# Optimization experiments

Measured on AMD Instinct MI355X. Metric: run time of the kernel, lower is better.

The kernel has to match this reference:

```python
import jax, jax.numpy as jnp
import numpy as np
import math

GROUPS = 32
HEADS = 8
EPS_GN = 1e-5


def group_norm(x, w, b):
    # x: [B, C, H, W]; GroupNorm32 computes in float32
    B, C, H, W = x.shape
    xg = x.astype(jnp.float32).reshape(B, GROUPS, C // GROUPS, H, W)
    mu = xg.mean(axis=(2, 3, 4), keepdims=True)
    var = xg.var(axis=(2, 3, 4), keepdims=True)
    xn = (xg - mu) * jax.lax.rsqrt(var + EPS_GN)
    xn = xn.reshape(B, C, H, W)
    return (xn * w[None, :, None, None] + b[None, :, None, None]).astype(x.dtype)


def fresnel_interference(H, W, wavelength):
    ys, xs = jnp.meshgrid(jnp.arange(H, dtype=jnp.float32),
                          jnp.arange(W, dtype=jnp.float32), indexing='ij')
    pos = jnp.stack([ys, xs], axis=-1).reshape(-1, 2)  # [N, 2]
    diff = pos[None, :, :] - pos[:, None, :]           # [N, N, 2]
    dist = jnp.sqrt((diff ** 2).sum(-1) + 1e-8)        # [N, N]
    phase = 2.0 * math.pi * dist / (jnp.abs(wavelength) * H + 1e-6)
    return jnp.cos(phase)


def fresnel_attn(h, qkv_w, out_w, out_b, wavelength):
    B, C, H, W = h.shape
    N = H * W
    dh = C // HEADS
    scale = dh ** -0.5
    xf = h.reshape(B, C, N).transpose(0, 2, 1)                 # [B, N, C]
    qkv = xf @ qkv_w                                            # [B, N, 3C]
    q, k, v = jnp.split(qkv, 3, axis=-1)
    def heads(t):
        return t.reshape(B, N, HEADS, dh).transpose(0, 2, 1, 3)  # [B, Hh, N, dh]
    q, k, v = heads(q), heads(k), heads(v)
    dots = jnp.einsum('bhnd,bhmd->bhnm', q, k) * scale
    interference = fresnel_interference(H, W, wavelength)       # [N, N]
    dots = dots + interference[None, None] * 0.1
    attn = jax.nn.softmax(dots, axis=-1)
    out = jnp.einsum('bhnm,bhmd->bhnd', attn, v)
    out = out.transpose(0, 2, 1, 3).reshape(B, N, C)
    out = out @ out_w + out_b
    return out.transpose(0, 2, 1).reshape(B, C, H, W)


def cross_attn(h, context, q_w, k_w, v_w, out_w, out_b):
    B, C, H, W = h.shape
    N = H * W
    inner = q_w.shape[1]
    dh = inner // HEADS
    scale = dh ** -0.5
    xf = h.reshape(B, C, N).transpose(0, 2, 1)                 # [B, N, C]
    q = xf @ q_w                                                # [B, N, inner]
    k = context @ k_w                                           # [B, L, inner]
    v = context @ v_w
    L = context.shape[1]
    q = q.reshape(B, N, HEADS, dh).transpose(0, 2, 1, 3)
    k = k.reshape(B, L, HEADS, dh).transpose(0, 2, 1, 3)
    v = v.reshape(B, L, HEADS, dh).transpose(0, 2, 1, 3)
    attn = jax.nn.softmax(jnp.einsum('bhnd,bhld->bhnl', q, k) * scale, axis=-1)
    out = jnp.einsum('bhnl,bhld->bhnd', attn, v)
    out = out.transpose(0, 2, 1, 3).reshape(B, N, inner)
    out = out @ out_w + out_b
    return out.transpose(0, 2, 1).reshape(B, C, H, W)


def setup_inputs() -> dict:
    key = jax.random.key(0)
    ks = jax.random.split(key, 10)
    B, C, H, W = 4, 512, 32, 32
    ctx_len, ctx_dim = 77, 768
    s = lambda d: 1.0 / math.sqrt(d)
    return {
        'x': jax.random.normal(ks[0], (B, C, H, W), jnp.float32),
        'context': jax.random.normal(ks[1], (B, ctx_len, ctx_dim), jnp.float32),
        'gn1_w': jnp.ones((C,), jnp.float32),
        'gn1_b': jnp.zeros((C,), jnp.float32),
        'gn2_w': jnp.ones((C,), jnp.float32),
        'gn2_b': jnp.zeros((C,), jnp.float32),
        'fa_qkv_w': jax.random.normal(ks[2], (C, 3 * C), jnp.float32) * s(C),
        'fa_out_w': jax.random.normal(ks[3], (C, C), jnp.float32) * s(C),
        'fa_out_b': jnp.zeros((C,), jnp.float32),
        'wavelength': jnp.asarray(0.1, jnp.float32),
        'ca_q_w': jax.random.normal(ks[4], (C, 512), jnp.float32) * s(C),
        'ca_k_w': jax.random.normal(ks[5], (ctx_dim, 512), jnp.float32) * s(ctx_dim),
        'ca_v_w': jax.random.normal(ks[6], (ctx_dim, 512), jnp.float32) * s(ctx_dim),
        'ca_out_w': jax.random.normal(ks[7], (512, C), jnp.float32) * s(512),
        'ca_out_b': jnp.zeros((C,), jnp.float32),
    }


def reference(x, context, gn1_w, gn1_b, gn2_w, gn2_b,
              fa_qkv_w, fa_out_w, fa_out_b, wavelength,
              ca_q_w, ca_k_w, ca_v_w, ca_out_w, ca_out_b):
    h = group_norm(x, gn1_w, gn1_b)
    h = fresnel_attn(h, fa_qkv_w, fa_out_w, fa_out_b, wavelength)
    x = x + h
    h = group_norm(x, gn2_w, gn2_b)
    h = cross_attn(h, context, ca_q_w, ca_k_w, ca_v_w, ca_out_w, ca_out_b)
    return x + h
```

## Files before the change

kernel.cpp:

```cpp
#include <hip/hip_runtime.h>
#include <hip/hip_bf16.h>
#include <math.h>

#define B_    4
#define N_    1024
#define L_    77

typedef float f4 __attribute__((ext_vector_type(4)));
typedef short bf8 __attribute__((ext_vector_type(8)));
typedef short s4v __attribute__((ext_vector_type(4)));

#if __has_builtin(__builtin_amdgcn_exp2f)
#define EXP2(x) __builtin_amdgcn_exp2f(x)
#else
#define EXP2(x) exp2f(x)
#endif

__device__ __forceinline__ float fs(short s) {
    unsigned u = ((unsigned)(unsigned short)s) << 16;
    return __builtin_bit_cast(float, u);
}
__device__ __forceinline__ short sf(float f) {
    unsigned u = __builtin_bit_cast(unsigned, f);
    unsigned r = (u + 0x7FFF + ((u >> 16) & 1)) >> 16;
    return (short)r;
}
__device__ __forceinline__ bf8 zero8() { bf8 v; for (int i = 0; i < 8; ++i) v[i] = 0; return v; }
__device__ __forceinline__ f4 zerof4() { f4 v; for (int i = 0; i < 4; ++i) v[i] = 0.f; return v; }

#define MFMA(a, b, c) __builtin_amdgcn_mfma_f32_16x16x32_bf16((a), (b), (c), 0, 0, 0)

__device__ __forceinline__ void gn_body(const float* __restrict__ src,
                                        const float* __restrict__ w,
                                        const float* __restrict__ bs,
                                        short* __restrict__ dst, int g, int b)
{
    const float* xb = src + ((size_t)b * 512 + g * 16) * 1024;
    float s = 0.f, ss = 0.f;
    for (int l = threadIdx.x; l < 4096; l += 256) {
        float4 v = *(const float4*)(xb + l * 4);
        s += v.x + v.y + v.z + v.w;
        ss += v.x * v.x + v.y * v.y + v.z * v.z + v.w * v.w;
    }
    for (int off = 32; off; off >>= 1) {
        s  += __shfl_down(s,  off);
        ss += __shfl_down(ss, off);
    }
    __shared__ float sred[8], ssred[8];
    int wid = threadIdx.x >> 6;
    if ((threadIdx.x & 63) == 0) { sred[wid] = s; ssred[wid] = ss; }
    __syncthreads();
    if (threadIdx.x == 0) {
        float S = 0.f, SS = 0.f;
        for (int i = 0; i < 4; ++i) { S += sred[i]; SS += ssred[i]; }
        float mu = S * (1.f / 16384.f);
        float var = SS * (1.f / 16384.f) - mu * mu;
        sred[4] = mu; ssred[4] = rsqrtf(var + 1e-5f);
    }
    __syncthreads();
    float mu = sred[4], rs = ssred[4];

    int c4 = threadIdx.x & 3, nb = threadIdx.x >> 2;
    int c = g * 16 + c4 * 4;
    float4 wv = *(const float4*)(w + c);
    float4 bv = *(const float4*)(bs + c);
    for (int rep = 0; rep < 16; ++rep) {
        int n = rep * 64 + nb;
        float v0 = xb[(size_t)(c4 * 4 + 0) * 1024 + n];
        float v1 = xb[(size_t)(c4 * 4 + 1) * 1024 + n];
        float v2 = xb[(size_t)(c4 * 4 + 2) * 1024 + n];
        float v3 = xb[(size_t)(c4 * 4 + 3) * 1024 + n];
        s4v hb;
        hb[0] = sf((v0 - mu) * rs * wv.x + bv.x);
        hb[1] = sf((v1 - mu) * rs * wv.y + bv.y);
        hb[2] = sf((v2 - mu) * rs * wv.z + bv.z);
        hb[3] = sf((v3 - mu) * rs * wv.w + bv.w);
        *(s4v*)(dst + ((size_t)b * 1024 + n) * 512 + c) = hb;
    }
}

__device__ __forceinline__ void wtile(const float* __restrict__ in, short* __restrict__ out,
                                      int K, int J, int tile, int tid, float (*t)[33])
{
    int jt = J >> 5;
    int j0 = (tile % jt) * 32, k0 = (tile / jt) * 32;
    int tx = tid & 31, ty = tid >> 5;
#pragma unroll
    for (int i = 0; i < 4; ++i)
        t[ty + i * 8][tx] = in[(size_t)(k0 + ty + i * 8) * J + j0 + tx];
    __syncthreads();
#pragma unroll
    for (int i = 0; i < 4; ++i)
        out[(size_t)(j0 + ty + i * 8) * K + k0 + tx] = sf(t[tx][ty + i * 8]);
}

__global__ __launch_bounds__(256)
void prep_mega(const float* __restrict__ x, const float* __restrict__ gn1w,
               const float* __restrict__ gn1b, short* __restrict__ h1b,
               const float* __restrict__ wl, short* __restrict__ tab,
               float* __restrict__ gstat,
               const float* __restrict__ qkvw, short* __restrict__ qkvwT,
               const float* __restrict__ faow, short* __restrict__ faowT,
               const float* __restrict__ caqw, short* __restrict__ caqwT,
               const float* __restrict__ cakw, short* __restrict__ cakwT,
               const float* __restrict__ cavw, short* __restrict__ cavwT,
               const float* __restrict__ caow, short* __restrict__ caowT,
               const float* __restrict__ ctx, short* __restrict__ ctxb)
{
    __shared__ float tls[32][33];
    int bid = blockIdx.x, tid = threadIdx.x;
    if (bid < 128) { gn_body(x, gn1w, gn1b, h1b, bid & 31, bid >> 5); return; }
    bid -= 128;
    if (bid < 16) {
        if (bid == 0) gstat[tid] = 0.f;
        int idx = bid * 256 + tid;
        if (idx < 3969) {
            int i = idx / 63, j = idx - i * 63;
            float dy = (float)(i - 31), dx = (float)(j - 31);
            float dist = sqrtf(dy * dy + dx * dx + 1e-8f);
            float den = fabsf(wl[0]) * 32.0f + 1e-6f;
            tab[idx] = sf(0.1f * cosf(6.283185307179586f * dist / den) * 1.4426950408889634f);
        }
        return;
    }
    bid -= 16;
    if (bid < 768) { wtile(qkvw, qkvwT, 512, 1536, bid, tid, tls); return; }
    bid -= 768;
    if (bid < 256) { wtile(faow, faowT, 512, 512, bid, tid, tls); return; }
    bid -= 256;
    if (bid < 256) { wtile(caqw, caqwT, 512, 512, bid, tid, tls); return; }
    bid -= 256;
    if (bid < 384) { wtile(cakw, cakwT, 768, 512, bid, tid, tls); return; }
    bid -= 384;
    if (bid < 384) { wtile(cavw, cavwT, 768, 512, bid, tid, tls); return; }
    bid -= 384;
    if (bid < 256) { wtile(caow, caowT, 512, 512, bid, tid, tls); return; }
    bid -= 256;
    int base = bid * 1024 + tid * 4;
    float4 v = *(const float4*)(ctx + base);
    s4v o; o[0] = sf(v.x); o[1] = sf(v.y); o[2] = sf(v.z); o[3] = sf(v.w);
    *(s4v*)(ctxb + base) = o;
}

__global__ __launch_bounds__(256)
void gn2_norm(const float* __restrict__ x1, const float* __restrict__ gstat,
              const float* __restrict__ w, const float* __restrict__ bs,
              short* __restrict__ dst)
{
    int g = blockIdx.x, b = blockIdx.y;
    float S  = gstat[b * 64 + g * 2];
    float SS = gstat[b * 64 + g * 2 + 1];
    float mu = S * (1.f / 16384.f);
    float var = SS * (1.f / 16384.f) - mu * mu;
    float rs = rsqrtf(var + 1e-5f);
    const float* xb = x1 + ((size_t)b * 512 + g * 16) * 1024;

    int c4 = threadIdx.x & 3, nb = threadIdx.x >> 2;
    int c = g * 16 + c4 * 4;
    float4 wv = *(const float4*)(w + c);
    float4 bv = *(const float4*)(bs + c);
    for (int rep = 0; rep < 16; ++rep) {
        int n = rep * 64 + nb;
        float v0 = xb[(size_t)(c4 * 4 + 0) * 1024 + n];
        float v1 = xb[(size_t)(c4 * 4 + 1) * 1024 + n];
        float v2 = xb[(size_t)(c4 * 4 + 2) * 1024 + n];
        float v3 = xb[(size_t)(c4 * 4 + 3) * 1024 + n];
        s4v hb;
        hb[0] = sf((v0 - mu) * rs * wv.x + bv.x);
        hb[1] = sf((v1 - mu) * rs * wv.y + bv.y);
        hb[2] = sf((v2 - mu) * rs * wv.z + bv.z);
        hb[3] = sf((v3 - mu) * rs * wv.w + bv.w);
        *(s4v*)(dst + ((size_t)b * 1024 + n) * 512 + c) = hb;
    }
}

template<int EPI>
__device__ __forceinline__ void gemm_body(
    short* As, short* Ws, int j0, int m0, int b,
    const short* __restrict__ A, const short* __restrict__ Wt,
    const float* __restrict__ bias, const float* __restrict__ res,
    void* __restrict__ outv, void* __restrict__ out2v, float* __restrict__ gstat,
    int M, int K, int J, long aStride, long wStride, long oStride, long o2Stride)
{
    int tid = threadIdx.x, w = tid >> 6, lane = tid & 63;
    int lr = lane & 15, lg = lane >> 4;
    int wr = w >> 1, wc = w & 1;
    const short* Ab  = A  + (size_t)b * aStride;
    const short* Wtb = Wt + (size_t)b * wStride;
    int r0 = tid >> 2, c0 = (tid & 3) * 8;
    bool gA0 = (m0 + r0) < M;
    const short* ap0 = Ab + (size_t)(m0 + r0) * K + c0;
    const short* wp0 = Wtb + (size_t)(j0 + r0) * K + c0;
    const short* wp1 = Wtb + (size_t)(j0 + 64 + r0) * K + c0;

    f4 acc[2][4];
#pragma unroll
    for (int i = 0; i < 2; ++i)
#pragma unroll
        for (int j = 0; j < 4; ++j) acc[i][j] = zerof4();

    *(bf8*)(As + r0 * 40 + c0) = gA0 ? *(const bf8*)ap0 : zero8();
    *(bf8*)(Ws + r0 * 40 + c0) = *(const bf8*)wp0;
    *(bf8*)(Ws + (64 + r0) * 40 + c0) = *(const bf8*)wp1;
    __syncthreads();

    int nk = K >> 5;
    for (int t = 0; t < nk; ++t) {
        int curA = (t & 1) * 2560, curW = (t & 1) * 5120;
        bool more = (t + 1) < nk;
        bf8 na0, nw0, nw1;
        if (more) {
            int ko = (t + 1) << 5;
            na0 = gA0 ? *(const bf8*)(ap0 + ko) : zero8();
            nw0 = *(const bf8*)(wp0 + ko);
            nw1 = *(const bf8*)(wp1 + ko);
        }
        bf8 af[2], bfr[4];
#pragma unroll
        for (int fi = 0; fi < 2; ++fi)
            af[fi] = *(const bf8*)(As + curA + (wr * 32 + fi * 16 + lr) * 40 + lg * 8);
#pragma unroll
        for (int fj = 0; fj < 4; ++fj)
            bfr[fj] = *(const bf8*)(Ws + curW + (wc * 64 + fj * 16 + lr) * 40 + lg * 8);
#pragma unroll
        for (int fi = 0; fi < 2; ++fi)
#pragma unroll
            for (int fj = 0; fj < 4; ++fj)
                acc[fi][fj] = MFMA(af[fi], bfr[fj], acc[fi][fj]);
        if (more) {
            int nbA = 2560 - curA, nbW = 5120 - curW;
            *(bf8*)(As + nbA + r0 * 40 + c0) = na0;
            *(bf8*)(Ws + nbW + r0 * 40 + c0) = nw0;
            *(bf8*)(Ws + nbW + (64 + r0) * 40 + c0) = nw1;
        }
        __syncthreads();
    }

    if (EPI == 1 || EPI == 2) {
        float* out = (float*)outv + (size_t)b * oStride;
        const float* rp = res + (size_t)b * oStride;
#pragma unroll
        for (int fi = 0; fi < 2; ++fi) {
            int mbase = m0 + wr * 32 + fi * 16 + lg * 4;
            float4 bq = *(const float4*)(bias + mbase);
            float bvr[4] = {bq.x, bq.y, bq.z, bq.w};
            float sg = 0.f, ssg = 0.f;
#pragma unroll
            for (int reg = 0; reg < 4; ++reg) {
                size_t ro = (size_t)(mbase + reg) * J + j0 + wc * 64;
#pragma unroll
                for (int fj = 0; fj < 4; ++fj) {
                    size_t idx = ro + fj * 16 + lr;
                    float v = acc[fi][fj][reg] + bvr[reg] + rp[idx];
                    out[idx] = v;
                    if (EPI == 2) { sg += v; ssg += v * v; }
                }
            }
            if (EPI == 2) {
#pragma unroll
                for (int off = 32; off; off >>= 1) {
                    sg  += __shfl_down(sg,  off);
                    ssg += __shfl_down(ssg, off);
                }
                if (lane == 0) {
                    int g = mbase >> 4;
                    atomicAdd(&gstat[b * 64 + g * 2], sg);
                    atomicAdd(&gstat[b * 64 + g * 2 + 1], ssg);
                }
            }
        }
    } else if (EPI == 3) {
        if (j0 < 1024) {
            short* out = (short*)outv + (size_t)b * oStride;
#pragma unroll
            for (int fi = 0; fi < 2; ++fi)
#pragma unroll
                for (int reg = 0; reg < 4; ++reg) {
                    int m = m0 + wr * 32 + fi * 16 + lg * 4 + reg;
#pragma unroll
                    for (int fj = 0; fj < 4; ++fj)
                        out[(size_t)m * 1024 + j0 + wc * 64 + fj * 16 + lr] = sf(acc[fi][fj][reg]);
                }
        } else {
            short* Vgp = (short*)out2v + (size_t)b * o2Stride;
#pragma unroll
            for (int fi = 0; fi < 2; ++fi) {
                int n = m0 + wr * 32 + fi * 16 + lg * 4;
#pragma unroll
                for (int fj = 0; fj < 4; ++fj) {
                    int dg = j0 - 1024 + wc * 64 + fj * 16 + lr;
                    s4v v;
#pragma unroll
                    for (int reg = 0; reg < 4; ++reg) v[reg] = sf(acc[fi][fj][reg]);
                    *(s4v*)(Vgp + (size_t)dg * 1024 + n) = v;
                }
            }
        }
    } else {
        if (j0 < 512) {
            short* out = (short*)outv + (size_t)b * oStride;
#pragma unroll
            for (int fi = 0; fi < 2; ++fi)
#pragma unroll
                for (int reg = 0; reg < 4; ++reg) {
                    int m = m0 + wr * 32 + fi * 16 + lg * 4 + reg;
                    if (m < M) {
#pragma unroll
                        for (int fj = 0; fj < 4; ++fj)
                            out[(size_t)m * 512 + j0 + wc * 64 + fj * 16 + lr] = sf(acc[fi][fj][reg]);
                    }
                }
        } else {
            short* vt = (short*)out2v + (size_t)b * o2Stride;
#pragma unroll
            for (int fi = 0; fi < 2; ++fi) {
                int l0 = m0 + wr * 32 + fi * 16 + lg * 4;
                if (l0 < 80) {
#pragma unroll
                    for (int fj = 0; fj < 4; ++fj) {
                        int dg = j0 - 512 + wc * 64 + fj * 16 + lr;
                        s4v v;
#pragma unroll
                        for (int reg = 0; reg < 4; ++reg) v[reg] = sf(acc[fi][fj][reg]);
                        *(s4v*)(vt + (size_t)dg * 80 + l0) = v;
                    }
                }
            }
        }
    }
}

template<int EPI>
__global__ __launch_bounds__(256)
void gemm_std(const short* __restrict__ A, const short* __restrict__ Wt,
              const float* __restrict__ bias, const float* __restrict__ res,
              void* __restrict__ outv, void* __restrict__ out2v, float* __restrict__ gstat,
              int M, int K, int J, long aStride, long wStride, long oStride, long o2Stride)
{
    __shared__ short As[2 * 64 * 40];
    __shared__ short Ws[2 * 128 * 40];
    gemm_body<EPI>(As, Ws, blockIdx.x * 128, blockIdx.y * 64, blockIdx.z,
                   A, Wt, bias, res, outv, out2v, gstat, M, K, J,
                   aStride, wStride, oStride, o2Stride);
}

__global__ __launch_bounds__(256)
void gemm_qkv_kv(const short* __restrict__ h1b, const short* __restrict__ qkvwT,
                 short* __restrict__ qkb, short* __restrict__ Vg,
                 const short* __restrict__ ctxb, const short* __restrict__ cakwT,
                 short* __restrict__ k2b, short* __restrict__ v2t)
{
    __shared__ short As[2 * 64 * 40];
    __shared__ short Ws[2 * 128 * 40];
    if (blockIdx.y < 16) {
        gemm_body<3>(As, Ws, blockIdx.x * 128, blockIdx.y * 64, blockIdx.z,
                     h1b, qkvwT, nullptr, nullptr, qkb, Vg, nullptr,
                     1024, 512, 1536, 524288L, 0L, 1048576L, 524288L);
    } else if (blockIdx.x < 8) {
        gemm_body<4>(As, Ws, blockIdx.x * 128, (blockIdx.y - 16) * 64, blockIdx.z,
                     ctxb, cakwT, nullptr, nullptr, k2b, v2t, nullptr,
                     77, 768, 1024, 59136L, 0L, 39424L, 40960L);
    }
}

__global__ __launch_bounds__(256)
void fresnel_attn_v3(const short* __restrict__ qkb, const short* __restrict__ Vg,
                     const short* __restrict__ tab, short* __restrict__ ao)
{
    int qb = blockIdx.x, h = blockIdx.y, b = blockIdx.z;
    int n0 = qb * 64;
    __shared__ short Ks[2][64][64];
    __shared__ short Vt[2][64][64];
    __shared__ short Ps[4][16][72];
    __shared__ short tabs[4032];
    int tid = threadIdx.x, w = tid >> 6, lane = tid & 63;
    int lr = lane & 15, lg = lane >> 4;
    const short* qp = qkb + (size_t)b * 1048576;
    const short* vp = Vg + ((size_t)b * 512 + h * 64) * 1024;

    for (int l = tid; l < 504; l += 256)
        *(bf8*)&tabs[l * 8] = *(const bf8*)(tab + l * 8);

    int q = n0 + w * 16 + lr;
    bf8 qf0 = *(const bf8*)(qp + (size_t)q * 1024 + h * 64 + lg * 8);
    bf8 qf1 = *(const bf8*)(qp + (size_t)q * 1024 + h * 64 + 32 + lg * 8);

    int sr0 = tid >> 3, sc0 = tid & 7;
    int sr1 = 32 + sr0;
    int sw0 = ((sc0 ^ (sr0 & 7))) * 8;
    int sw1 = ((sc0 ^ (sr1 & 7))) * 8;

    *(bf8*)&Ks[0][sr0][sw0] = *(const bf8*)(qp + (size_t)sr0 * 1024 + 512 + h * 64 + sc0 * 8);
    *(bf8*)&Ks[0][sr1][sw1] = *(const bf8*)(qp + (size_t)sr1 * 1024 + 512 + h * 64 + sc0 * 8);
    *(bf8*)&Vt[0][sr0][sw0] = *(const bf8*)(vp + (size_t)sr0 * 1024 + sc0 * 8);
    *(bf8*)&Vt[0][sr1][sw1] = *(const bf8*)(vp + (size_t)sr1 * 1024 + sc0 * 8);
    __syncthreads();

    float mrun = -1e30f, lrun = 0.f;
    f4 o[4];
#pragma unroll
    for (int i = 0; i < 4; ++i) o[i] = zerof4();

    int ybase = (q >> 5) + 31;
    int xbase = (q & 31) + 31 - lg * 4;
    int rsw = lr & 7;
    int rc0 = (lg ^ rsw) * 8;
    int rc1 = ((4 + lg) ^ rsw) * 8;

    for (int t = 0; t < 16; ++t) {
        int cur = t & 1;
        int m0 = t << 6;
        bool more = t < 15;
        bf8 nk0, nk1, nv0, nv1;
        if (more) {
            int m1 = m0 + 64;
            nk0 = *(const bf8*)(qp + (size_t)(m1 + sr0) * 1024 + 512 + h * 64 + sc0 * 8);
            nk1 = *(const bf8*)(qp + (size_t)(m1 + sr1) * 1024 + 512 + h * 64 + sc0 * 8);
            nv0 = *(const bf8*)(vp + (size_t)sr0 * 1024 + m1 + sc0 * 8);
            nv1 = *(const bf8*)(vp + (size_t)sr1 * 1024 + m1 + sc0 * 8);
        }

        f4 sa[4];
#pragma unroll
        for (int fj = 0; fj < 4; ++fj) sa[fj] = zerof4();
        __builtin_amdgcn_s_setprio(1);
#pragma unroll
        for (int fj = 0; fj < 4; ++fj)
            sa[fj] = MFMA(*(const bf8*)&Ks[cur][fj * 16 + lr][rc0], qf0, sa[fj]);
#pragma unroll
        for (int fj = 0; fj < 4; ++fj)
            sa[fj] = MFMA(*(const bf8*)&Ks[cur][fj * 16 + lr][rc1], qf1, sa[fj]);
        __builtin_amdgcn_s_setprio(0);

        int yb = ybase - (m0 >> 5);
        float pv[4][4];
        float tmax = -1e30f;
#pragma unroll
        for (int fj = 0; fj < 4; ++fj) {
            int rowoff = (yb - (fj >> 1)) * 63 + xbase - (fj & 1) * 16;
#pragma unroll
            for (int reg = 0; reg < 4; ++reg) {
                float t2 = fmaf(sa[fj][reg], 0.18033688011112042f, fs(tabs[rowoff - reg]));
                pv[fj][reg] = t2;
                tmax = fmaxf(tmax, t2);
            }
        }
        if (__any(tmax > mrun + 8.f)) {
            tmax = fmaxf(tmax, __shfl_xor(tmax, 16));
            tmax = fmaxf(tmax, __shfl_xor(tmax, 32));
            float mnew = fmaxf(mrun, tmax);
            float rsc = EXP2(mrun - mnew);
            mrun = mnew;
            lrun *= rsc;
#pragma unroll
            for (int fd = 0; fd < 4; ++fd)
#pragma unroll
                for (int reg = 0; reg < 4; ++reg) o[fd][reg] *= rsc;
        }
        float psum = 0.f;
#pragma unroll
        for (int fj = 0; fj < 4; ++fj) {
            float p0 = EXP2(pv[fj][0] - mrun);
            float p1 = EXP2(pv[fj][1] - mrun);
            float p2 = EXP2(pv[fj][2] - mrun);
            float p3 = EXP2(pv[fj][3] - mrun);
            psum += (p0 + p1) + (p2 + p3);
            int r01, r23;
            asm("v_cvt_pk_bf16_f32 %0, %1, %2" : "=v"(r01) : "v"(p0), "v"(p1));
            asm("v_cvt_pk_bf16_f32 %0, %1, %2" : "=v"(r23) : "v"(p2), "v"(p3));
            int2 pr; pr.x = r01; pr.y = r23;
            *(int2*)&Ps[w][lr][fj * 16 + lg * 4] = pr;
        }
        psum += __shfl_xor(psum, 16);
        psum += __shfl_xor(psum, 32);
        lrun += psum;

        bf8 pa0 = *(const bf8*)&Ps[w][lr][lg * 8];
        bf8 pa1 = *(const bf8*)&Ps[w][lr][32 + lg * 8];
        __builtin_amdgcn_s_setprio(1);
#pragma unroll
        for (int fd = 0; fd < 4; ++fd) {
            o[fd] = MFMA(*(const bf8*)&Vt[cur][fd * 16 + lr][rc0], pa0, o[fd]);
            o[fd] = MFMA(*(const bf8*)&Vt[cur][fd * 16 + lr][rc1], pa1, o[fd]);
        }
        __builtin_amdgcn_s_setprio(0);

        if (more) {
            int nb = cur ^ 1;
            *(bf8*)&Ks[nb][sr0][sw0] = nk0;
            *(bf8*)&Ks[nb][sr1][sw1] = nk1;
            *(bf8*)&Vt[nb][sr0][sw0] = nv0;
            *(bf8*)&Vt[nb][sr1][sw1] = nv1;
        }
        __syncthreads();
    }

    float inv = 1.f / lrun;
    size_t rb = ((size_t)b * N_ + q) * 512 + h * 64;
#pragma unroll
    for (int fd = 0; fd < 4; ++fd) {
        s4v ov;
#pragma unroll
        for (int reg = 0; reg < 4; ++reg) ov[reg] = sf(o[fd][reg] * inv);
        *(s4v*)(ao + rb + fd * 16 + lg * 4) = ov;
    }
}

__global__ __launch_bounds__(256)
void cross_attn_fused(const short* __restrict__ h2, const short* __restrict__ qwT,
                      const short* __restrict__ k2, const short* __restrict__ v2t,
                      short* __restrict__ ao2)
{
    int qb = blockIdx.x, h = blockIdx.y, b = blockIdx.z;
    int n0 = qb * 64;
    __shared__ short hq[2][64][40], wq[2][64][40];
    __shared__ short Qs[64][72], Ks[96][72], Vt[64][104];
    __shared__ short Ps[4][16][104];
    int tid = threadIdx.x, w = tid >> 6, lane = tid & 63;
    int lr = lane & 15, lg = lane >> 4;

    for (int l = tid; l < 768; l += 256) {
        int m = l >> 3, dq = l & 7;
        bf8 v = zero8();
        if (m < L_) v = *(const bf8*)(k2 + ((size_t)b * L_ + m) * 512 + h * 64 + dq * 8);
        *(bf8*)&Ks[m][dq * 8] = v;
    }
    for (int l = tid; l < 768; l += 256) {
        int d = l / 12, cq = l % 12;
        bf8 v = zero8();
        if (cq < 10) v = *(const bf8*)(v2t + ((size_t)b * 512 + h * 64 + d) * 80 + cq * 8);
        *(bf8*)&Vt[d][cq * 8] = v;
    }

    int r0 = tid >> 2, c0 = (tid & 3) * 8;
    const short* hp = h2 + ((size_t)b * 1024 + n0 + r0) * 512 + c0;
    const short* wp = qwT + (size_t)(h * 64 + r0) * 512 + c0;
    *(bf8*)&hq[0][r0][c0] = *(const bf8*)hp;
    *(bf8*)&wq[0][r0][c0] = *(const bf8*)wp;
    __syncthreads();

    f4 qacc[4];
#pragma unroll
    for (int j = 0; j < 4; ++j) qacc[j] = zerof4();
    for (int t = 0; t < 16; ++t) {
        int cur = t & 1;
        bool more = t < 15;
        bf8 nh, nw;
        if (more) {
            int ko = (t + 1) << 5;
            nh = *(const bf8*)(hp + ko);
            nw = *(const bf8*)(wp + ko);
        }
        bf8 af = *(const bf8*)&hq[cur][w * 16 + lr][lg * 8];
#pragma unroll
        for (int fj = 0; fj < 4; ++fj)
            qacc[fj] = MFMA(af, *(const bf8*)&wq[cur][fj * 16 + lr][lg * 8], qacc[fj]);
        if (more) {
            int nb = cur ^ 1;
            *(bf8*)&hq[nb][r0][c0] = nh;
            *(bf8*)&wq[nb][r0][c0] = nw;
        }
        __syncthreads();
    }
#pragma unroll
    for (int fj = 0; fj < 4; ++fj)
#pragma unroll
        for (int reg = 0; reg < 4; ++reg)
            Qs[w * 16 + lg * 4 + reg][fj * 16 + lr] = sf(qacc[fj][reg]);
    __syncthreads();

    f4 sacc[6];
#pragma unroll
    for (int fj = 0; fj < 6; ++fj) sacc[fj] = zerof4();
    __builtin_amdgcn_s_setprio(1);
#pragma unroll
    for (int kc = 0; kc < 2; ++kc) {
        bf8 aq = *(const bf8*)&Qs[w * 16 + lr][kc * 32 + lg * 8];
#pragma unroll
        for (int fj = 0; fj < 6; ++fj)
            sacc[fj] = MFMA(aq, *(const bf8*)&Ks[fj * 16 + lr][kc * 32 + lg * 8], sacc[fj]);
    }
    __builtin_amdgcn_s_setprio(0);

    float rinv[4];
#pragma unroll
    for (int reg = 0; reg < 4; ++reg) {
        float sv[6];
#pragma unroll
        for (int fj = 0; fj < 6; ++fj) {
            int m = fj * 16 + lr;
            sv[fj] = (m < L_) ? sacc[fj][reg] * 0.125f : -30000.f;
        }
        float mx = sv[0];
#pragma unroll
        for (int fj = 1; fj < 6; ++fj) mx = fmaxf(mx, sv[fj]);
#pragma unroll
        for (int off = 1; off < 16; off <<= 1) mx = fmaxf(mx, __shfl_xor(mx, off));
        float psum = 0.f;
#pragma unroll
        for (int fj = 0; fj < 6; ++fj) {
            float p = __expf(sv[fj] - mx);
            psum += p;
            Ps[w][lg * 4 + reg][fj * 16 + lr] = sf(p);
        }
#pragma unroll
        for (int off = 1; off < 16; off <<= 1) psum += __shfl_xor(psum, off);
        rinv[reg] = 1.f / psum;
    }
    __syncthreads();

    f4 o[4];
#pragma unroll
    for (int fd = 0; fd < 4; ++fd) o[fd] = zerof4();
    __builtin_amdgcn_s_setprio(1);
#pragma unroll
    for (int kc = 0; kc < 3; ++kc) {
        bf8 ap = *(const bf8*)&Ps[w][lr][kc * 32 + lg * 8];
#pragma unroll
        for (int fd = 0; fd < 4; ++fd)
            o[fd] = MFMA(ap, *(const bf8*)&Vt[fd * 16 + lr][kc * 32 + lg * 8], o[fd]);
    }
    __builtin_amdgcn_s_setprio(0);

#pragma unroll
    for (int reg = 0; reg < 4; ++reg) {
        size_t rb = ((size_t)b * N_ + n0 + w * 16 + lg * 4 + reg) * 512 + h * 64;
#pragma unroll
        for (int fd = 0; fd < 4; ++fd)
            ao2[rb + fd * 16 + lr] = sf(o[fd][reg] * rinv[reg]);
    }
}

extern "C" void kernel_launch(void* const* d_in, const int* in_sizes, int n_in,
                              void* d_out, int out_size, void* d_ws, size_t ws_size,
                              hipStream_t stream)
{
    const float* x    = (const float*)d_in[0];
    const float* ctx  = (const float*)d_in[1];
    const float* gn1w = (const float*)d_in[2];
    const float* gn1b = (const float*)d_in[3];
    const float* gn2w = (const float*)d_in[4];
    const float* gn2b = (const float*)d_in[5];
    const float* qkvw = (const float*)d_in[6];
    const float* faow = (const float*)d_in[7];
    const float* faob = (const float*)d_in[8];
    const float* wl   = (const float*)d_in[9];
    const float* caqw = (const float*)d_in[10];
    const float* cakw = (const float*)d_in[11];
    const float* cavw = (const float*)d_in[12];
    const float* caow = (const float*)d_in[13];
    const float* caob = (const float*)d_in[14];
    float* out = (float*)d_out;
    char* ws = (char*)d_ws;

    float* x1    = (float*)(ws + 0);
    short* qkb   = (short*)(ws + 8388608);
    short* Vg    = (short*)(ws + 16777216);
    short* h1b   = (short*)(ws + 20971520);
    short* ao    = (short*)(ws + 25165824);
    float* gstat = (float*)(ws + 29360128);
    short* qkvwT = (short*)(ws + 33554432);
    short* faowT = (short*)(ws + 35127296);
    short* caqwT = (short*)(ws + 35651584);
    short* cakwT = (short*)(ws + 36175872);
    short* cavwT = (short*)(ws + 36962304);
    short* caowT = (short*)(ws + 37748736);
    short* k2b   = (short*)(ws + 38273024);
    short* v2t   = (short*)(ws + 38588416);
    short* ctxb  = (short*)(ws + 38916096);
    short* tab   = (short*)(ws + 39389184);

    prep_mega<<<2679, 256, 0, stream>>>(x, gn1w, gn1b, h1b,
                                        wl, tab, gstat, qkvw, qkvwT, faow, faowT,
                                        caqw, caqwT, cakw, cakwT, cavw, cavwT,
                                        caow, caowT, ctx, ctxb);
    gemm_qkv_kv<<<dim3(12, 18, 4), 256, 0, stream>>>(
        h1b, qkvwT, qkb, Vg, ctxb, cakwT, k2b, v2t);
    fresnel_attn_v3<<<dim3(16, 8, 4), 256, 0, stream>>>(qkb, Vg, tab, ao);
    gemm_std<2><<<dim3(8, 8, 4), 256, 0, stream>>>(
        faowT, ao, faob, x, x1, nullptr, gstat, 512, 512, 1024,
        0L, 524288L, 524288L, 0L);
    gn2_norm<<<dim3(32, 4), 256, 0, stream>>>(x1, gstat, gn2w, gn2b, h1b);
    cross_attn_fused<<<dim3(16, 8, 4), 256, 0, stream>>>(h1b, caqwT, k2b, v2t, ao);
    gemm_std<1><<<dim3(8, 8, 4), 256, 0, stream>>>(
        caowT, ao, caob, x1, out, nullptr, nullptr, 512, 512, 1024,
        0L, 524288L, 524288L, 0L);
}
```

Measured before the change: 201.4 us.

## Use direct global-to-LDS loads in GEMMs and fuse GroupNorm2 into cross-attention

```diff
diff --git a/kernel.cpp b/kernel.cpp
--- a/kernel.cpp
+++ b/kernel.cpp
@@ -15,6 +15,10 @@
 #else
 #define EXP2(x) exp2f(x)
 #endif
+
+typedef const __attribute__((address_space(1))) void* gas_t;
+typedef __attribute__((address_space(3))) void* las_t;
+#define GLL16(g, l) __builtin_amdgcn_global_load_lds((gas_t)(const void*)(g), (las_t)(void*)(l), 16, 0, 0)
 
 __device__ __forceinline__ float fs(short s) {
     unsigned u = ((unsigned)(unsigned short)s) << 16;
@@ -142,38 +146,6 @@
     *(s4v*)(ctxb + base) = o;
 }
 
-__global__ __launch_bounds__(256)
-void gn2_norm(const float* __restrict__ x1, const float* __restrict__ gstat,
-              const float* __restrict__ w, const float* __restrict__ bs,
-              short* __restrict__ dst)
-{
-    int g = blockIdx.x, b = blockIdx.y;
-    float S  = gstat[b * 64 + g * 2];
-    float SS = gstat[b * 64 + g * 2 + 1];
-    float mu = S * (1.f / 16384.f);
-    float var = SS * (1.f / 16384.f) - mu * mu;
-    float rs = rsqrtf(var + 1e-5f);
-    const float* xb = x1 + ((size_t)b * 512 + g * 16) * 1024;
-
-    int c4 = threadIdx.x & 3, nb = threadIdx.x >> 2;
-    int c = g * 16 + c4 * 4;
-    float4 wv = *(const float4*)(w + c);
-    float4 bv = *(const float4*)(bs + c);
-    for (int rep = 0; rep < 16; ++rep) {
-        int n = rep * 64 + nb;
-        float v0 = xb[(size_t)(c4 * 4 + 0) * 1024 + n];
-        float v1 = xb[(size_t)(c4 * 4 + 1) * 1024 + n];
-        float v2 = xb[(size_t)(c4 * 4 + 2) * 1024 + n];
-        float v3 = xb[(size_t)(c4 * 4 + 3) * 1024 + n];
-        s4v hb;
-        hb[0] = sf((v0 - mu) * rs * wv.x + bv.x);
-        hb[1] = sf((v1 - mu) * rs * wv.y + bv.y);
-        hb[2] = sf((v2 - mu) * rs * wv.z + bv.z);
-        hb[3] = sf((v3 - mu) * rs * wv.w + bv.w);
-        *(s4v*)(dst + ((size_t)b * 1024 + n) * 512 + c) = hb;
-    }
-}
-
 template<int EPI>
 __device__ __forceinline__ void gemm_body(
     short* As, short* Ws, int j0, int m0, int b,
@@ -187,11 +159,14 @@
     int wr = w >> 1, wc = w & 1;
     const short* Ab  = A  + (size_t)b * aStride;
     const short* Wtb = Wt + (size_t)b * wStride;
-    int r0 = tid >> 2, c0 = (tid & 3) * 8;
-    bool gA0 = (m0 + r0) < M;
-    const short* ap0 = Ab + (size_t)(m0 + r0) * K + c0;
-    const short* wp0 = Wtb + (size_t)(j0 + r0) * K + c0;
-    const short* wp1 = Wtb + (size_t)(j0 + 64 + r0) * K + c0;
+
+    int srow = lane >> 2, schk = (lane & 3) * 8;
+    const short* agp  = Ab  + (size_t)(m0 + w * 16 + srow) * K + schk;
+    const short* wgp0 = Wtb + (size_t)(j0 + w * 32 + srow) * K + schk;
+    const short* wgp1 = Wtb + (size_t)(j0 + w * 32 + 16 + srow) * K + schk;
+    short* alp  = As + w * 512;
+    short* wlp0 = Ws + w * 1024;
+    short* wlp1 = Ws + w * 1024 + 512;
 
     f4 acc[2][4];
 #pragma unroll
@@ -199,40 +174,32 @@
 #pragma unroll
         for (int j = 0; j < 4; ++j) acc[i][j] = zerof4();
 
-    *(bf8*)(As + r0 * 40 + c0) = gA0 ? *(const bf8*)ap0 : zero8();
-    *(bf8*)(Ws + r0 * 40 + c0) = *(const bf8*)wp0;
-    *(bf8*)(Ws + (64 + r0) * 40 + c0) = *(const bf8*)wp1;
+    GLL16(agp,  alp);
+    GLL16(wgp0, wlp0);
+    GLL16(wgp1, wlp1);
     __syncthreads();
 
     int nk = K >> 5;
     for (int t = 0; t < nk; ++t) {
-        int curA = (t & 1) * 2560, curW = (t & 1) * 5120;
-        bool more = (t + 1) < nk;
-        bf8 na0, nw0, nw1;
-        if (more) {
+        int bb = t & 1, nb2 = bb ^ 1;
+        if (t + 1 < nk) {
             int ko = (t + 1) << 5;
-            na0 = gA0 ? *(const bf8*)(ap0 + ko) : zero8();
-            nw0 = *(const bf8*)(wp0 + ko);
-            nw1 = *(const bf8*)(wp1 + ko);
+            GLL16(agp + ko,  alp + nb2 * 2048);
+            GLL16(wgp0 + ko, wlp0 + nb2 * 4096);
+            GLL16(wgp1 + ko, wlp1 + nb2 * 4096);
         }
         bf8 af[2], bfr[4];
 #pragma unroll
         for (int fi = 0; fi < 2; ++fi)
-            af[fi] = *(const bf8*)(As + curA + (wr * 32 + fi * 16 + lr) * 40 + lg * 8);
+            af[fi] = *(const bf8*)(As + bb * 2048 + (wr * 32 + fi * 16 + lr) * 32 + lg * 8);
 #pragma unroll
         for (int fj = 0; fj < 4; ++fj)
-            bfr[fj] = *(const bf8*)(Ws + curW + (wc * 64 + fj * 16 + lr) * 40 + lg * 8);
+            bfr[fj] = *(const bf8*)(Ws + bb * 4096 + (wc * 64 + fj * 16 + lr) * 32 + lg * 8);
 #pragma unroll
         for (int fi = 0; fi < 2; ++fi)
 #pragma unroll
             for (int fj = 0; fj < 4; ++fj)
                 acc[fi][fj] = MFMA(af[fi], bfr[fj], acc[fi][fj]);
-        if (more) {
-            int nbA = 2560 - curA, nbW = 5120 - curW;
-            *(bf8*)(As + nbA + r0 * 40 + c0) = na0;
-            *(bf8*)(Ws + nbW + r0 * 40 + c0) = nw0;
-            *(bf8*)(Ws + nbW + (64 + r0) * 40 + c0) = nw1;
-        }
         __syncthreads();
     }
 
@@ -337,8 +304,8 @@
               void* __restrict__ outv, void* __restrict__ out2v, float* __restrict__ gstat,
               int M, int K, int J, long aStride, long wStride, long oStride, long o2Stride)
 {
-    __shared__ short As[2 * 64 * 40];
-    __shared__ short Ws[2 * 128 * 40];
+    __shared__ short As[2 * 64 * 32];
+    __shared__ short Ws[2 * 128 * 32];
     gemm_body<EPI>(As, Ws, blockIdx.x * 128, blockIdx.y * 64, blockIdx.z,
                    A, Wt, bias, res, outv, out2v, gstat, M, K, J,
                    aStride, wStride, oStride, o2Stride);
@@ -350,8 +317,8 @@
                  const short* __restrict__ ctxb, const short* __restrict__ cakwT,
                  short* __restrict__ k2b, short* __restrict__ v2t)
 {
-    __shared__ short As[2 * 64 * 40];
-    __shared__ short Ws[2 * 128 * 40];
+    __shared__ short As[2 * 64 * 32];
+    __shared__ short Ws[2 * 128 * 32];
     if (blockIdx.y < 16) {
         gemm_body<3>(As, Ws, blockIdx.x * 128, blockIdx.y * 64, blockIdx.z,
                      h1b, qkvwT, nullptr, nullptr, qkb, Vg, nullptr,
@@ -507,17 +474,30 @@
 }
 
 __global__ __launch_bounds__(256)
-void cross_attn_fused(const short* __restrict__ h2, const short* __restrict__ qwT,
+void cross_attn_fused(const float* __restrict__ x1, const float* __restrict__ gstat,
+                      const float* __restrict__ gn2w, const float* __restrict__ gn2b,
+                      const short* __restrict__ qwT,
                       const short* __restrict__ k2, const short* __restrict__ v2t,
                       short* __restrict__ ao2)
 {
     int qb = blockIdx.x, h = blockIdx.y, b = blockIdx.z;
     int n0 = qb * 64;
-    __shared__ short hq[2][64][40], wq[2][64][40];
+    __shared__ short hq[2][64][40];
+    __shared__ short wq[2 * 64 * 32];
     __shared__ short Qs[64][72], Ks[96][72], Vt[64][104];
     __shared__ short Ps[4][16][104];
+    __shared__ float smu[32], srs[32];
     int tid = threadIdx.x, w = tid >> 6, lane = tid & 63;
     int lr = lane & 15, lg = lane >> 4;
+
+    if (tid < 32) {
+        float S  = gstat[b * 64 + tid * 2];
+        float SS = gstat[b * 64 + tid * 2 + 1];
+        float mu = S * (1.f / 16384.f);
+        float var = SS * (1.f / 16384.f) - mu * mu;
+        smu[tid] = mu;
+        srs[tid] = rsqrtf(var + 1e-5f);
+    }
 
     for (int l = tid; l < 768; l += 256) {
         int m = l >> 3, dq = l & 7;
@@ -532,33 +512,64 @@
         *(bf8*)&Vt[d][cq * 8] = v;
     }
 
-    int r0 = tid >> 2, c0 = (tid & 3) * 8;
-    const short* hp = h2 + ((size_t)b * 1024 + n0 + r0) * 512 + c0;
-    const short* wp = qwT + (size_t)(h * 64 + r0) * 512 + c0;
-    *(bf8*)&hq[0][r0][c0] = *(const bf8*)hp;
-    *(bf8*)&wq[0][r0][c0] = *(const bf8*)wp;
+    int srow = lane >> 2, schk = (lane & 3) * 8;
+    const short* wgp = qwT + (size_t)(h * 64 + w * 16 + srow) * 512 + schk;
+    short* wlp = wq + w * 512;
+
+    int cr = tid >> 4, cn = (tid & 15) * 4;
+    const float* xp0 = x1 + ((size_t)b * 512 + cr) * 1024 + n0 + cn;
+    const float* xp1 = xp0 + 16 * 1024;
+
+    GLL16(wgp, wlp);
+    float4 f0 = *(const float4*)(xp0);
+    float4 f1 = *(const float4*)(xp1);
+    float wv0 = gn2w[cr],      bv0 = gn2b[cr];
+    float wv1 = gn2w[cr + 16], bv1 = gn2b[cr + 16];
+    __syncthreads();
+    {
+        float mu0 = smu[0], rs0 = srs[0];
+        float mu1 = smu[1], rs1 = srs[1];
+        float a0 = rs0 * wv0, a1 = rs1 * wv1;
+        float c0 = bv0 - mu0 * a0, c1 = bv1 - mu1 * a1;
+#pragma unroll
+        for (int i = 0; i < 4; ++i) {
+            hq[0][cn + i][cr]      = sf(f0[i] * a0 + c0);
+            hq[0][cn + i][cr + 16] = sf(f1[i] * a1 + c1);
+        }
+    }
     __syncthreads();
 
     f4 qacc[4];
 #pragma unroll
     for (int j = 0; j < 4; ++j) qacc[j] = zerof4();
     for (int t = 0; t < 16; ++t) {
-        int cur = t & 1;
+        int cur = t & 1, nb = cur ^ 1;
         bool more = t < 15;
-        bf8 nh, nw;
+        float4 nf0, nf1;
+        float nw0, nb0, nw1, nb1;
         if (more) {
             int ko = (t + 1) << 5;
-            nh = *(const bf8*)(hp + ko);
-            nw = *(const bf8*)(wp + ko);
+            GLL16(wgp + ko, wlp + nb * 2048);
+            nf0 = *(const float4*)(xp0 + ko * 1024);
+            nf1 = *(const float4*)(xp1 + ko * 1024);
+            nw0 = gn2w[ko + cr];      nb0 = gn2b[ko + cr];
+            nw1 = gn2w[ko + cr + 16]; nb1 = gn2b[ko + cr + 16];
         }
         bf8 af = *(const bf8*)&hq[cur][w * 16 + lr][lg * 8];
 #pragma unroll
         for (int fj = 0; fj < 4; ++fj)
-            qacc[fj] = MFMA(af, *(const bf8*)&wq[cur][fj * 16 + lr][lg * 8], qacc[fj]);
+            qacc[fj] = MFMA(af, *(const bf8*)(wq + cur * 2048 + (fj * 16 + lr) * 32 + lg * 8), qacc[fj]);
         if (more) {
-            int nb = cur ^ 1;
-            *(bf8*)&hq[nb][r0][c0] = nh;
-            *(bf8*)&wq[nb][r0][c0] = nw;
+            int g0 = (t + 1) * 2, g1 = g0 + 1;
+            float mu0 = smu[g0], rs0 = srs[g0];
+            float mu1 = smu[g1], rs1 = srs[g1];
+            float a0 = rs0 * nw0, a1 = rs1 * nw1;
+            float c0 = nb0 - mu0 * a0, c1 = nb1 - mu1 * a1;
+#pragma unroll
+            for (int i = 0; i < 4; ++i) {
+                hq[nb][cn + i][cr]      = sf(nf0[i] * a0 + c0);
+                hq[nb][cn + i][cr + 16] = sf(nf1[i] * a1 + c1);
+            }
         }
         __syncthreads();
     }
@@ -680,8 +691,8 @@
     gemm_std<2><<<dim3(8, 8, 4), 256, 0, stream>>>(
         faowT, ao, faob, x, x1, nullptr, gstat, 512, 512, 1024,
         0L, 524288L, 524288L, 0L);
-    gn2_norm<<<dim3(32, 4), 256, 0, stream>>>(x1, gstat, gn2w, gn2b, h1b);
-    cross_attn_fused<<<dim3(16, 8, 4), 256, 0, stream>>>(h1b, caqwT, k2b, v2t, ao);
+    cross_attn_fused<<<dim3(16, 8, 4), 256, 0, stream>>>(
+        x1, gstat, gn2w, gn2b, caqwT, k2b, v2t, ao);
     gemm_std<1><<<dim3(8, 8, 4), 256, 0, stream>>>(
         caowT, ao, caob, x1, out, nullptr, nullptr, 512, 512, 1024,
         0L, 524288L, 524288L, 0L);
```

After: 203.1 us. Within noise of the previous version (+0.9%).
